# Performance work log

Measured on AMD Instinct MI355X. Metric: run time of the kernel, lower is better.

Reference implementation:

```python
import jax, jax.numpy as jnp
import numpy as np

NC, NPR, E, B = 200000, 100000, 500000, 200000
DIN, HID, HEADS = 16, 256, 8
D = HID // HEADS
NCOLOR, NSIZE, NGROUP = 1000, 30, 50


def setup_inputs() -> dict:
    key = jax.random.key(0)
    ks = jax.random.split(key, 24)
    g = lambda i, shape, s=0.05: jax.random.normal(ks[i], shape, jnp.float32) * s
    return dict(
        customer_x=g(0, (NC, DIN), 1.0),
        product_x=g(1, (NPR, DIN), 1.0),
        proj_cust_W=g(2, (DIN, HID)), proj_cust_b=jnp.zeros((HID,), jnp.float32),
        proj_prod_W=g(3, (DIN, HID)), proj_prod_b=jnp.zeros((HID,), jnp.float32),
        att_src_r=g(4, (HEADS, D)), att_dst_r=g(5, (HEADS, D)),
        att_src_rb=g(6, (HEADS, D)), att_dst_rb=g(7, (HEADS, D)),
        q_sem=g(8, (HID,)), k_lin_W=g(9, (HID, HID)), k_lin_b=jnp.zeros((HID,), jnp.float32),
        color_emb=g(10, (NCOLOR, 8), 1.0),
        size_emb=g(11, (NSIZE, 4), 1.0),
        group_emb=g(12, (NGROUP, 4), 1.0),
        fc1_W=g(13, (HID * 2 + 16, 128)), fc1_b=jnp.zeros((128,), jnp.float32),
        fc2_W=g(14, (128, 32)), fc2_b=jnp.zeros((32,), jnp.float32),
        fc3_W=g(15, (32, 1)), fc3_b=jnp.zeros((1,), jnp.float32),
        bn1_gamma=jnp.ones((128,), jnp.float32), bn1_beta=jnp.zeros((128,), jnp.float32),
        bn2_gamma=jnp.ones((32,), jnp.float32), bn2_beta=jnp.zeros((32,), jnp.float32),
        edge_src=jax.random.randint(ks[16], (E,), 0, NC),
        edge_dst=jax.random.randint(ks[17], (E,), 0, NPR),
        label_src=jax.random.randint(ks[18], (B,), 0, NC),
        label_dst=jax.random.randint(ks[19], (B,), 0, NPR),
        size_idx=jax.random.randint(ks[20], (B,), 0, NSIZE),
        color_idx=jax.random.randint(ks[21], (B,), 0, NCOLOR),
        group_idx=jax.random.randint(ks[22], (B,), 0, NGROUP),
    )


def _edge_softmax(logits, dst, n):
    # destination-grouped softmax over edges; logits: [E,H]
    m = jax.ops.segment_max(logits, dst, num_segments=n)
    m = jnp.where(jnp.isfinite(m), m, 0.0)
    e = jnp.exp(logits - m[dst])
    s = jax.ops.segment_sum(e, dst, num_segments=n)
    return e / (s[dst] + 1e-16)


def _han_relation(h_src, h_dst, a_src, a_dst, src, dst, n_dst):
    # h_*: [N,H,D]; a_*: [H,D]
    logits = (h_src * a_src).sum(-1)[src] + (h_dst * a_dst).sum(-1)[dst]  # [E,H]
    logits = jax.nn.leaky_relu(logits, 0.2)
    alpha = _edge_softmax(logits, dst, n_dst)
    msg = alpha[:, :, None] * h_src[src]  # [E,H,D]
    out = jax.ops.segment_sum(msg, dst, num_segments=n_dst)
    return jax.nn.relu(out.reshape(n_dst, -1))  # [N_dst, H*D]


def _group(outs, q, kW, kb):
    # semantic attention over metapaths (PyG HANConv group)
    stk = jnp.stack(outs)  # [M,N,F]
    score = (q * jnp.tanh(stk @ kW + kb).mean(1)).sum(-1)  # [M]
    attn = jax.nn.softmax(score)
    return jnp.einsum('m,mnf->nf', attn, stk)


def _bn(x, gamma, beta):
    mu = x.mean(0)
    var = x.var(0)
    return (x - mu) * jax.lax.rsqrt(var + 1e-5) * gamma + beta


def reference(customer_x, product_x, proj_cust_W, proj_cust_b, proj_prod_W, proj_prod_b,
              att_src_r, att_dst_r, att_src_rb, att_dst_rb, q_sem, k_lin_W, k_lin_b,
              color_emb, size_emb, group_emb, fc1_W, fc1_b, fc2_W, fc2_b, fc3_W, fc3_b,
              bn1_gamma, bn1_beta, bn2_gamma, bn2_beta,
              edge_src, edge_dst, label_src, label_dst, size_idx, color_idx, group_idx):
    h_c = (customer_x @ proj_cust_W + proj_cust_b).reshape(-1, HEADS, D)
    h_p = (product_x @ proj_prod_W + proj_prod_b).reshape(-1, HEADS, D)
    # relation customer -returns-> product
    out_p = _han_relation(h_c, h_p, att_src_r, att_dst_r, edge_src, edge_dst, NPR)
    # relation product -returned_by-> customer (reversed edges)
    out_c = _han_relation(h_p, h_c, att_src_rb, att_dst_rb, edge_dst, edge_src, NC)
    cust = _group([out_c], q_sem, k_lin_W, k_lin_b)  # [NC, 256]
    prod = _group([out_p], q_sem, k_lin_W, k_lin_b)  # [NPR, 256]
    feat = jnp.concatenate([cust[label_src], prod[label_dst],
                            size_emb[size_idx], color_emb[color_idx], group_emb[group_idx]], axis=-1)
    x = jax.nn.relu(feat @ fc1_W + fc1_b)
    x = _bn(x, bn1_gamma, bn1_beta)
    x = jax.nn.relu(x @ fc2_W + fc2_b)
    x = _bn(x, bn2_gamma, bn2_beta)
    return x @ fc3_W + fc3_b
```

## Files before the change

### kernel.cpp

```cpp
#include <hip/hip_runtime.h>

#define NCC 200000
#define NPRR 100000
#define NEE 500000
#define NBB 200000
#define CAPP 96000
#define CAPC 160000

typedef __attribute__((ext_vector_type(8))) short bf16x8;
typedef __attribute__((ext_vector_type(16))) float f32x16;

__device__ __forceinline__ float b2f(unsigned short u){ return __uint_as_float(((unsigned)u)<<16); }
__device__ __forceinline__ unsigned short f2b(float f){
  unsigned x = __float_as_uint(f);
  return (unsigned short)((x + 0x7fffu + ((x>>16)&1u)) >> 16);
}


__global__ __launch_bounds__(256) void wa_prep2(
    const float* __restrict__ Wc, const float* __restrict__ bc,
    const float* __restrict__ attAc, const float* __restrict__ attBc,
    const float* __restrict__ Wp, const float* __restrict__ bp,
    const float* __restrict__ attAp, const float* __restrict__ attBp,
    float* __restrict__ WAc, float* __restrict__ WAp)
{
  int tid = threadIdx.x;
  for (int task = tid; task < 4*17*8; task += 256) {
    int grp = task / 136, rem = task % 136;
    int k = rem >> 3, h = rem & 7;
    const float* att = (grp==0)?attAc:(grp==1)?attBc:(grp==2)?attAp:attBp;
    const float* W   = (grp<2)?Wc:Wp;
    const float* bias= (grp<2)?bc:bp;
    const float* row = (k < 16) ? (W + k*256) : bias;
    float acc = 0.f;
    for (int d = 0; d < 32; d++) acc = fmaf(row[h*32+d], att[h*32+d], acc);
    if (grp<2) WAc[(grp&1)*136 + rem] = acc;
    else       WAp[(grp&1)*136 + rem] = acc;
  }
}

__global__ __launch_bounds__(256) void prep_proj(
    const float* __restrict__ Wc, const float* __restrict__ Wp,
    const float* __restrict__ WAc, const float* __restrict__ WAp,
    unsigned short* __restrict__ WtC, unsigned short* __restrict__ WtP,
    unsigned short* __restrict__ WAtC, unsigned short* __restrict__ WAtP)
{
  int idx = blockIdx.x*256 + threadIdx.x;
  if (idx < 4096){ int n=idx>>4, k=idx&15; WtC[idx]=f2b(Wc[k*256+n]); }
  else if (idx < 8192){ int t=idx-4096; int n=t>>4, k=t&15; WtP[t]=f2b(Wp[k*256+n]); }
  else if (idx < 8704){ int t=idx-8192; int n=t>>4, k=t&15;
    WAtC[t] = (n<16)? f2b(WAc[(n>>3)*136 + k*8 + (n&7)]) : (unsigned short)0; }
  else if (idx < 9216){ int t=idx-8704; int n=t>>4, k=t&15;
    WAtP[t] = (n<16)? f2b(WAp[(n>>3)*136 + k*8 + (n&7)]) : (unsigned short)0; }
}

__global__ __launch_bounds__(256) void prep_fc1(const float* __restrict__ fc1W,
    const float* __restrict__ fc1b,
    const float* __restrict__ size_emb, const float* __restrict__ color_emb,
    const float* __restrict__ group_emb,
    unsigned short* __restrict__ BtC, unsigned short* __restrict__ BtP,
    float* __restrict__ Ts, float* __restrict__ Tc, float* __restrict__ Tg)
{
  int idx = blockIdx.x*256 + threadIdx.x;
  if (idx < 32768){
    int n = idx>>8, k = idx&255;
    BtC[idx] = f2b(fc1W[k*128 + n]);
  } else if (idx < 65536){
    int t = idx - 32768;
    int n = t>>8, k = t&255;
    BtP[t] = f2b(fc1W[(256+k)*128 + n]);
  } else if (idx < 65536 + 30*128){
    int t = idx - 65536;
    int s = t>>7, j = t&127;
    float a = fc1b[j];
    #pragma unroll
    for (int c=0;c<4;c++) a = fmaf(size_emb[s*4+c], fc1W[(512+c)*128+j], a);
    Ts[t] = a;
  } else if (idx < 65536 + 30*128 + 1000*128){
    int t = idx - 65536 - 30*128;
    int col = t>>7, j = t&127;
    float a = 0.f;
    #pragma unroll
    for (int c=0;c<8;c++) a = fmaf(color_emb[col*8+c], fc1W[(516+c)*128+j], a);
    Tc[t] = a;
  } else if (idx < 65536 + 30*128 + 1000*128 + 50*128){
    int t = idx - 65536 - 30*128 - 1000*128;
    int g = t>>7, j = t&127;
    float a = 0.f;
    #pragma unroll
    for (int c=0;c<4;c++) a = fmaf(group_emb[g*4+c], fc1W[(524+c)*128+j], a);
    Tg[t] = a;
  }
}

#define PROJ_NB 2048
__global__ __launch_bounds__(256) void proj_hist(const float* __restrict__ X,
    const unsigned short* __restrict__ Wt, const unsigned short* __restrict__ WAt,
    const float* __restrict__ WA,
    unsigned short* __restrict__ H, float* __restrict__ sA, float* __restrict__ sB,
    int nt, int nHist,
    const int* __restrict__ src, const int* __restrict__ dst,
    int* __restrict__ cnt_c, int* __restrict__ cnt_p, int E,
    const int* __restrict__ lsrc, const int* __restrict__ ldst,
    int* __restrict__ used_c, int* __restrict__ used_p, int B)
{
  __shared__ unsigned short wt[4608];
  __shared__ float biasS[16];
  int tid = threadIdx.x;
  int bid = blockIdx.x;
  int both = 2*nHist;
  bool isHist; int rid;
  if (bid < both){ isHist = (bid & 1); rid = bid >> 1; }
  else           { isHist = false;    rid = nHist + (bid - both); }
  if (isHist){
    int e = rid*256 + tid;
    if (e < E){
      atomicAdd(&cnt_p[dst[e]], 1);
      atomicAdd(&cnt_c[src[e]], 1);
    }
    if (e < B){
      used_c[lsrc[e]] = 1;
      used_p[ldst[e]] = 1;
    }
    return;
  }
  for (int i=tid; i<512; i+=256) ((uint4*)wt)[i] = ((const uint4*)Wt)[i];
  for (int i=tid; i<64;  i+=256) ((uint4*)(wt+4096))[i] = ((const uint4*)WAt)[i];
  if (tid < 16) biasS[tid] = WA[(tid>>3)*136 + 128 + (tid&7)];
  __syncthreads();
  int wv = tid>>6, lane = tid&63, m = lane&31, hi = lane>>5;
  for (int t = rid; t < nt; t += PROJ_NB){
    int node = t*32 + m;
    bf16x8 a;
    {
      const float4* xr = (const float4*)(X + (long long)node*16 + hi*8);
      float4 f0 = xr[0], f1 = xr[1];
      unsigned short av[8] = {f2b(f0.x),f2b(f0.y),f2b(f0.z),f2b(f0.w),
                              f2b(f1.x),f2b(f1.y),f2b(f1.z),f2b(f1.w)};
      a = *(bf16x8*)av;
    }
    #pragma unroll
    for (int s=0;s<2;s++){
      int c0 = wv*64 + s*32;
      bf16x8 b = *(const bf16x8*)(wt + (c0+m)*16 + hi*8);
      f32x16 acc;
      #pragma unroll
      for (int i=0;i<16;i++) acc[i]=0.f;
      acc = __builtin_amdgcn_mfma_f32_32x32x16_bf16(a, b, acc, 0, 0, 0);
      #pragma unroll
      for (int reg=0; reg<16; reg++){
        int row = (reg&3) + 8*(reg>>2) + 4*hi;
        H[(long long)(t*32+row)*256 + c0 + m] = f2b(acc[reg]);
      }
    }
    if (wv == 0){
      bf16x8 b = *(const bf16x8*)(wt + 4096 + m*16 + hi*8);
      f32x16 acc;
      #pragma unroll
      for (int i=0;i<16;i++) acc[i]=0.f;
      acc = __builtin_amdgcn_mfma_f32_32x32x16_bf16(a, b, acc, 0, 0, 0);
      if (m < 16){
        float bias = biasS[m];
        float* dst2 = (m < 8) ? sA : sB;
        int h = m & 7;
        #pragma unroll
        for (int reg=0; reg<16; reg++){
          int row = (reg&3) + 8*(reg>>2) + 4*hi;
          dst2[(long long)(t*32+row)*8 + h] = acc[reg] + bias;
        }
      }
    }
  }
}

__global__ __launch_bounds__(256) void scan_p1f(const int* __restrict__ cnt_p, int* __restrict__ bsum_p, int Np,
    const int* __restrict__ cnt_c, int* __restrict__ bsum_c, int Nc, int BP, int BC,
    const int* __restrict__ used_p, const int* __restrict__ used_c, int* __restrict__ L, int nComp)
{
  __shared__ int red[256];
  __shared__ int hcnt[16];
  int tid = threadIdx.x;
  int bid = blockIdx.x;
  if (bid >= BP + BC){
    int blk2 = bid - (BP + BC);
    int n = blk2*256 + tid;
    if (tid < 16) hcnt[tid] = 0;
    __syncthreads();
    if (n < Np && used_p[n]){
      int b = min((cnt_p[n]+3)>>2, 7);
      atomicAdd(&hcnt[b], 1);
    }
    if (n < Nc && used_c[n]){
      int b = min((cnt_c[n]+3)>>2, 7);
      atomicAdd(&hcnt[8+b], 1);
    }
    __syncthreads();
    if (tid < 8       && hcnt[tid])  atomicAdd(&L[8+tid],      hcnt[tid]);
    else if (tid < 16 && hcnt[tid])  atomicAdd(&L[16+(tid-8)], hcnt[tid]);
    return;
  }
  const int* cnt; int* bsum; int N; int blk;
  if (bid < BP){ cnt=cnt_p; bsum=bsum_p; N=Np; blk=bid; }
  else         { cnt=cnt_c; bsum=bsum_c; N=Nc; blk=bid-BP; }
  int base = blk*1024 + tid*4;
  int s = 0;
  #pragma unroll
  for (int k=0;k<4;k++){ int i=base+k; if (i<N) s += cnt[i]; }
  red[tid] = s;
  __syncthreads();
  for (int off=128; off>0; off>>=1){ if (tid<off) red[tid]+=red[tid+off]; __syncthreads(); }
  if (tid==0) bsum[blk] = red[0];
}

__global__ __launch_bounds__(256) void scan_p2f(int* __restrict__ bsum_p, int Bp, int* __restrict__ rowptr_p, int Np,
    int* __restrict__ bsum_c, int Bc, int* __restrict__ rowptr_c, int Nc, int* __restrict__ L)
{
  __shared__ int ts[256];
  int tid = threadIdx.x;
  if (blockIdx.x == 2){
    if (tid == 0){
      int s = 0;
      #pragma unroll
      for (int b=0;b<8;b++){ L[24+b] = s; s += L[8+b]; }
      L[0] = s;
      s = 0;
      #pragma unroll
      for (int b=0;b<8;b++){ L[32+b] = s; s += L[16+b]; }
      L[1] = s;
    }
    return;
  }
  int* bsum; int B; int* rowptr; int N;
  if (blockIdx.x == 0){ bsum=bsum_p; B=Bp; rowptr=rowptr_p; N=Np; }
  else                { bsum=bsum_c; B=Bc; rowptr=rowptr_c; N=Nc; }
  int v = (tid<B) ? bsum[tid] : 0;
  ts[tid] = v;
  __syncthreads();
  for (int off=1; off<256; off<<=1){
    int t = (tid>=off) ? ts[tid-off] : 0;
    __syncthreads();
    ts[tid] += t;
    __syncthreads();
  }
  if (tid < B) bsum[tid] = ts[tid] - v;
  if (tid == B-1) rowptr[N] = ts[tid];
}

__global__ __launch_bounds__(256) void scan_p3f(const int* __restrict__ cnt_p, const int* __restrict__ bsum_p,
    int* __restrict__ rowptr_p, int Np,
    const int* __restrict__ cnt_c, const int* __restrict__ bsum_c,
    int* __restrict__ rowptr_c, int Nc, int BP)
{
  __shared__ int ts[256];
  const int* cnt; const int* bsum; int* rowptr; int N; int blk;
  if ((int)blockIdx.x < BP){ cnt=cnt_p; bsum=bsum_p; rowptr=rowptr_p; N=Np; blk=blockIdx.x; }
  else                     { cnt=cnt_c; bsum=bsum_c; rowptr=rowptr_c; N=Nc; blk=blockIdx.x-BP; }
  int tid = threadIdx.x;
  int base = blk*1024 + tid*4;
  int v[4]; int s = 0;
  #pragma unroll
  for (int k=0;k<4;k++){ int i=base+k; v[k] = (i<N) ? cnt[i] : 0; s += v[k]; }
  ts[tid] = s;
  __syncthreads();
  for (int off=1; off<256; off<<=1){
    int t = (tid>=off) ? ts[tid-off] : 0;
    __syncthreads();
    ts[tid] += t;
    __syncthreads();
  }
  int run = bsum[blk] + ts[tid] - s;
  #pragma unroll
  for (int k=0;k<4;k++){ int i=base+k; if (i<N){ rowptr[i]=run; run += v[k]; } }
}

__global__ __launch_bounds__(256) void mega2(
    const int* __restrict__ src, const int* __restrict__ dst,
    const int* __restrict__ rp_r, const int* __restrict__ rp_rb,
    int* __restrict__ cnt_p2, int* __restrict__ cnt_c2,
    int* __restrict__ si_r, int* __restrict__ si_rb, int E,
    const int* __restrict__ used_p, const int* __restrict__ rowptr_p, int Np,
    int4* __restrict__ list_p, int* __restrict__ L, int* __restrict__ smap_p,
    const int* __restrict__ used_c, const int* __restrict__ rowptr_c, int Nc,
    int4* __restrict__ list_c, int* __restrict__ smap_c,
    int nComp,
    const float* __restrict__ X, const unsigned short* __restrict__ Wt,
    const unsigned short* __restrict__ WAt, const float* __restrict__ WA,
    unsigned short* __restrict__ H, float* __restrict__ sA, float* __restrict__ sB,
    int nt, int nProj)
{
  __shared__ unsigned short wt[4608];
  __shared__ float biasS[16];
  __shared__ int hcnt[16];
  __shared__ int hbase[16];
  __shared__ int hcur[16];
  int tid = threadIdx.x, bid = blockIdx.x;
  int nB = nComp + nProj;
  int both = 2*nB;
  bool isB; int rid;
  if (bid < both){ isB = (bid & 1); rid = bid >> 1; }
  else           { isB = false;     rid = nB + (bid - both); }
  if (isB){
    if (rid < nComp){
      int n = rid*256 + tid;
      if (tid < 16){ hcnt[tid] = 0; hcur[tid] = 0; }
      __syncthreads();
      int bp = -1, bc = -1;
      int e0p=0,e1p=0,e0c=0,e1c=0;
      if (n < Np && used_p[n]){
        e0p = rowptr_p[n]; e1p = rowptr_p[n+1];
        bp = min(((e1p-e0p)+3)>>2, 7);
        atomicAdd(&hcnt[bp], 1);
      }
      if (n < Nc && used_c[n]){
        e0c = rowptr_c[n]; e1c = rowptr_c[n+1];
        bc = min(((e1c-e0c)+3)>>2, 7);
        atomicAdd(&hcnt[8+bc], 1);
      }
      __syncthreads();
      if (tid < 8)        hbase[tid] = hcnt[tid] ? atomicAdd(&L[64+tid],     hcnt[tid]) : 0;
      else if (tid < 16)  hbase[tid] = hcnt[tid] ? atomicAdd(&L[72+(tid-8)], hcnt[tid]) : 0;
      __syncthreads();
      if (bp >= 0){
        int r = atomicAdd(&hcur[bp], 1);
        int slot = L[24+bp] + hbase[bp] + r;
        if (slot < CAPP){ list_p[slot] = make_int4(n, e0p, e1p, 0); smap_p[n] = slot; }
      }
      if (bc >= 0){
        int r = atomicAdd(&hcur[8+bc], 1);
        int slot = L[32+bc] + hbase[8+bc] + r;
        if (slot < CAPC){ list_c[slot] = make_int4(n, e0c, e1c, 0); smap_c[n] = slot; }
      }
      return;
    }
    int pid = rid - nComp;
    for (int i=tid; i<512; i+=256) ((uint4*)wt)[i] = ((const uint4*)Wt)[i];
    for (int i=tid; i<64;  i+=256) ((uint4*)(wt+4096))[i] = ((const uint4*)WAt)[i];
    if (tid < 16) biasS[tid] = WA[(tid>>3)*136 + 128 + (tid&7)];
    __syncthreads();
    int wv = tid>>6, lane = tid&63, m = lane&31, hi = lane>>5;
    for (int t = pid; t < nt; t += nProj){
      int node = t*32 + m;
      bf16x8 a;
      {
        const float4* xr = (const float4*)(X + (long long)node*16 + hi*8);
        float4 f0 = xr[0], f1 = xr[1];
        unsigned short av[8] = {f2b(f0.x),f2b(f0.y),f2b(f0.z),f2b(f0.w),
                                f2b(f1.x),f2b(f1.y),f2b(f1.z),f2b(f1.w)};
        a = *(bf16x8*)av;
      }
      #pragma unroll
      for (int s=0;s<2;s++){
        int c0 = wv*64 + s*32;
        bf16x8 b = *(const bf16x8*)(wt + (c0+m)*16 + hi*8);
        f32x16 acc;
        #pragma unroll
        for (int i=0;i<16;i++) acc[i]=0.f;
        acc = __builtin_amdgcn_mfma_f32_32x32x16_bf16(a, b, acc, 0, 0, 0);
        #pragma unroll
        for (int reg=0; reg<16; reg++){
          int row = (reg&3) + 8*(reg>>2) + 4*hi;
          H[(long long)(t*32+row)*256 + c0 + m] = f2b(acc[reg]);
        }
      }
      if (wv == 0){
        bf16x8 b = *(const bf16x8*)(wt + 4096 + m*16 + hi*8);
        f32x16 acc;
        #pragma unroll
        for (int i=0;i<16;i++) acc[i]=0.f;
        acc = __builtin_amdgcn_mfma_f32_32x32x16_bf16(a, b, acc, 0, 0, 0);
        if (m < 16){
          float bias = biasS[m];
          float* dst2 = (m < 8) ? sA : sB;
          int h = m & 7;
          #pragma unroll
          for (int reg=0; reg<16; reg++){
            int row = (reg&3) + 8*(reg>>2) + 4*hi;
            dst2[(long long)(t*32+row)*8 + h] = acc[reg] + bias;
          }
        }
      }
    }
    return;
  }
  int e = rid*256 + tid;
  if (e < E){
    int s = src[e], d = dst[e];
    si_r [rp_r [d] + atomicAdd(&cnt_p2[d], 1)] = s;
    si_rb[rp_rb[s] + atomicAdd(&cnt_c2[s], 1)] = d;
  }
}

__device__ __forceinline__ void agg_block(
    const int4* __restrict__ list, int cnt, int base,
    const int* __restrict__ srcidx,
    const float* __restrict__ sSrc, const float* __restrict__ sDst,
    const unsigned short* __restrict__ H, const unsigned short* __restrict__ Bt,
    unsigned short* __restrict__ Y, int tid, unsigned short* feat)
{
  int wv = tid>>6, lane = tid&63;
  int g = lane>>4, ln = lane&15, h = ln>>1;
  #pragma unroll
  for (int t=0;t<2;t++){
    int r = wv*8 + t*4 + g;
    int slot = base + r;
    float acc[16];
    #pragma unroll
    for (int c=0;c<16;c++) acc[c]=0.f;
    float den = 0.f;
    int node = -1, e0 = 0, e1 = 0;
    if (slot < cnt){
      int4 L = list[slot];
      node = L.x; e0 = L.y; e1 = L.z;
    }
    if (node >= 0 && e1 > e0){
      int elast = e1 - 1;
      float sdh = sDst[(long long)node*8 + h];
      for (int e = e0; e < e1; e += 4){
        int i1 = min(e+1, elast), i2 = min(e+2, elast), i3 = min(e+3, elast);
        int s0 = srcidx[e],  s1 = srcidx[i1];
        int s2 = srcidx[i2], s3 = srcidx[i3];
        const uint4* p0 = (const uint4*)&H[(long long)s0*256 + ln*16];
        const uint4* p1 = (const uint4*)&H[(long long)s1*256 + ln*16];
        const uint4* p2 = (const uint4*)&H[(long long)s2*256 + ln*16];
        const uint4* p3 = (const uint4*)&H[(long long)s3*256 + ln*16];
        uint4 uA0 = p0[0], uA1 = p0[1];
        uint4 uB0 = p1[0], uB1 = p1[1];
        uint4 uC0 = p2[0], uC1 = p2[1];
        uint4 uD0 = p3[0], uD1 = p3[1];
        float l0 = sSrc[(long long)s0*8 + h];
        float l1 = sSrc[(long long)s1*8 + h];
        float l2 = sSrc[(long long)s2*8 + h];
        float l3 = sSrc[(long long)s3*8 + h];
        l0 += sdh; l1 += sdh; l2 += sdh; l3 += sdh;
        float w0 = __expf(l0 > 0.f ? l0 : 0.2f*l0);
        float w1 = (e+1 < e1) ? __expf(l1 > 0.f ? l1 : 0.2f*l1) : 0.f;
        float w2 = (e+2 < e1) ? __expf(l2 > 0.f ? l2 : 0.2f*l2) : 0.f;
        float w3 = (e+3 < e1) ? __expf(l3 > 0.f ? l3 : 0.2f*l3) : 0.f;
        den += (w0 + w1) + (w2 + w3);
        unsigned ua[8] = {uA0.x,uA0.y,uA0.z,uA0.w, uA1.x,uA1.y,uA1.z,uA1.w};
        unsigned ub[8] = {uB0.x,uB0.y,uB0.z,uB0.w, uB1.x,uB1.y,uB1.z,uB1.w};
        unsigned uc[8] = {uC0.x,uC0.y,uC0.z,uC0.w, uC1.x,uC1.y,uC1.z,uC1.w};
        unsigned ud[8] = {uD0.x,uD0.y,uD0.z,uD0.w, uD1.x,uD1.y,uD1.z,uD1.w};
        #pragma unroll
        for (int p=0;p<8;p++){
          acc[p*2]   = fmaf(w0, b2f((unsigned short)(ua[p]&0xffffu)), acc[p*2]);
          acc[p*2+1] = fmaf(w0, b2f((unsigned short)(ua[p]>>16)),     acc[p*2+1]);
          acc[p*2]   = fmaf(w1, b2f((unsigned short)(ub[p]&0xffffu)), acc[p*2]);
          acc[p*2+1] = fmaf(w1, b2f((unsigned short)(ub[p]>>16)),     acc[p*2+1]);
          acc[p*2]   = fmaf(w2, b2f((unsigned short)(uc[p]&0xffffu)), acc[p*2]);
          acc[p*2+1] = fmaf(w2, b2f((unsigned short)(uc[p]>>16)),     acc[p*2+1]);
          acc[p*2]   = fmaf(w3, b2f((unsigned short)(ud[p]&0xffffu)), acc[p*2]);
          acc[p*2+1] = fmaf(w3, b2f((unsigned short)(ud[p]>>16)),     acc[p*2+1]);
        }
      }
    }
    float inv = 1.f/(den + 1e-16f);
    unsigned short ov[16];
    #pragma unroll
    for (int c=0;c<16;c++) ov[c] = f2b(fmaxf(acc[c]*inv, 0.f));
    *(uint4*)&feat[r*264 + ln*16]     = *(uint4*)&ov[0];
    *(uint4*)&feat[r*264 + ln*16 + 8] = *(uint4*)&ov[8];
  }
  __syncthreads();
  int m = lane&31, hi = lane>>5;
  f32x16 acc;
  #pragma unroll
  for (int i=0;i<16;i++) acc[i]=0.f;
  const unsigned short* ap  = feat + m*264 + hi*8;
  const unsigned short* btp = Bt + (wv*32 + m)*256 + hi*8;
  #pragma unroll 4
  for (int ks=0; ks<16; ks++){
    bf16x8 a = *(const bf16x8*)(ap + ks*16);
    bf16x8 b = *(const bf16x8*)(btp + ks*16);
    acc = __builtin_amdgcn_mfma_f32_32x32x16_bf16(a, b, acc, 0, 0, 0);
  }
  int col = wv*32 + m;
  #pragma unroll
  for (int reg=0; reg<16; reg++){
    int row = (reg&3) + 8*(reg>>2) + 4*hi;
    Y[(long long)(base+row)*128 + col] = f2b(acc[reg]);
  }
}

__global__ __launch_bounds__(256) void agg2(
    const int4* __restrict__ listP, const int* __restrict__ lcntP,
    const int* __restrict__ siR,
    const float* __restrict__ sCr, const float* __restrict__ sPr,
    const unsigned short* __restrict__ Hc, const unsigned short* __restrict__ BtP,
    unsigned short* __restrict__ YP, int nP,
    const int4* __restrict__ listC, const int* __restrict__ lcntC,
    const int* __restrict__ siRB,
    const float* __restrict__ sPrb, const float* __restrict__ sCrb,
    const unsigned short* __restrict__ Hp, const unsigned short* __restrict__ BtC,
    unsigned short* __restrict__ YC)
{
  __shared__ unsigned short feat[32*264];
  int bid = blockIdx.x, tid = threadIdx.x;
  int both = 2*nP;
  bool isR; int rid;
  if (bid < both){ isR = !(bid & 1); rid = bid >> 1; }
  else           { isR = false;      rid = nP + (bid - both); }
  if (isR){
    int cnt = *lcntP;
    int base = rid*32;
    if (base >= cnt) return;
    agg_block(listP, cnt, base, siR, sCr, sPr, Hc, BtP, YP, tid, feat);
  } else {
    int cnt = *lcntC;
    int base = rid*32;
    if (base >= cnt) return;
    agg_block(listC, cnt, base, siRB, sPrb, sCrb, Hp, BtC, YC, tid, feat);
  }
}

__global__ __launch_bounds__(256) void gather_fc1(
    const unsigned short* __restrict__ Yc, const unsigned short* __restrict__ Yp,
    const int* __restrict__ smap_c, const int* __restrict__ smap_p,
    const float* __restrict__ Ts, const float* __restrict__ Tc, const float* __restrict__ Tg,
    const int* __restrict__ lsrc, const int* __restrict__ ldst,
    const int* __restrict__ sidx, const int* __restrict__ cidx, const int* __restrict__ gidx,
    unsigned short* __restrict__ x1, float* __restrict__ bnsum, int ntiles)
{
  __shared__ float redS[16][128];
  __shared__ float redQ[16][128];
  int tid = threadIdx.x;
  int rl = tid>>4, g = tid&15;
  float sacc[8] = {0,0,0,0,0,0,0,0};
  float qacc[8] = {0,0,0,0,0,0,0,0};
  for (int t = blockIdx.x; t < ntiles; t += gridDim.x){
    long long row = (long long)t*16 + rl;
    int ls = smap_c[lsrc[row]], ld = smap_p[ldst[row]];
    int si = sidx[row], ci = cidx[row], gi = gidx[row];
    uint4 uc = *(const uint4*)&Yc[(long long)ls*128 + g*8];
    uint4 up = *(const uint4*)&Yp[(long long)ld*128 + g*8];
    float4 t0 = *(const float4*)&Ts[si*128 + g*8];
    float4 t1 = *(const float4*)&Ts[si*128 + g*8 + 4];
    float4 c0 = *(const float4*)&Tc[ci*128 + g*8];
    float4 c1 = *(const float4*)&Tc[ci*128 + g*8 + 4];
    float4 g0 = *(const float4*)&Tg[gi*128 + g*8];
    float4 g1 = *(const float4*)&Tg[gi*128 + g*8 + 4];
    unsigned ucs[4] = {uc.x,uc.y,uc.z,uc.w};
    unsigned ups[4] = {up.x,up.y,up.z,up.w};
    float tb[8] = {t0.x+c0.x+g0.x, t0.y+c0.y+g0.y, t0.z+c0.z+g0.z, t0.w+c0.w+g0.w,
                   t1.x+c1.x+g1.x, t1.y+c1.y+g1.y, t1.z+c1.z+g1.z, t1.w+c1.w+g1.w};
    unsigned short ov[8];
    #pragma unroll
    for (int p=0;p<4;p++){
      float vl = b2f((unsigned short)(ucs[p]&0xffffu)) + b2f((unsigned short)(ups[p]&0xffffu)) + tb[p*2];
      float vh = b2f((unsigned short)(ucs[p]>>16))     + b2f((unsigned short)(ups[p]>>16))     + tb[p*2+1];
      vl = fmaxf(vl, 0.f); vh = fmaxf(vh, 0.f);
      ov[p*2] = f2b(vl); ov[p*2+1] = f2b(vh);
      sacc[p*2]   += vl; qacc[p*2]   += vl*vl;
      sacc[p*2+1] += vh; qacc[p*2+1] += vh*vh;
    }
    *(uint4*)&x1[row*128 + g*8] = *(uint4*)ov;
  }
  #pragma unroll
  for (int j=0;j<8;j++){ redS[rl][g*8+j]=sacc[j]; redQ[rl][g*8+j]=qacc[j]; }
  __syncthreads();
  if (tid < 128){
    float s=0.f, q=0.f;
    #pragma unroll
    for (int r=0;r<16;r++){ s += redS[r][tid]; q += redQ[r][tid]; }
    atomicAdd(&bnsum[tid], s);
    atomicAdd(&bnsum[128+tid], q);
  }
}

__global__ void bn1_fold(const float* __restrict__ bnsum,
    const float* __restrict__ gamma, const float* __restrict__ beta,
    const float* __restrict__ fc2W, const float* __restrict__ fc2b,
    unsigned short* __restrict__ Bt2, float* __restrict__ b2p, float invB)
{
  __shared__ float sc[128], sh[128];
  int tid = threadIdx.x;
  if (tid<128){
    float mu  = bnsum[tid]*invB;
    float var = bnsum[128+tid]*invB - mu*mu;
    float s = gamma[tid] * rsqrtf(var + 1e-5f);
    sc[tid]=s; sh[tid]= beta[tid] - mu*s;
  }
  __syncthreads();
  for (int idx=tid; idx<32*128; idx+=256){
    int n = idx>>7, k = idx&127;
    Bt2[idx] = f2b(sc[k]*fc2W[k*32+n]);
  }
  if (tid<32){
    float a = fc2b[tid];
    for (int k=0;k<128;k++) a = fmaf(sh[k], fc2W[k*32+tid], a);
    b2p[tid]=a;
  }
}

__global__ __launch_bounds__(256) void fc2_mfma(const unsigned short* __restrict__ x1,
    const unsigned short* __restrict__ Bt2, const float* __restrict__ b2p,
    unsigned short* __restrict__ x2, float* __restrict__ bnsum2, int M)
{
  __shared__ unsigned short xt[128*136];
  __shared__ unsigned short wt[32*136];
  __shared__ float redS[4][32];
  __shared__ float redQ[4][32];
  int tid = threadIdx.x;
  long long base = (long long)blockIdx.x*128;
  for (int idx=tid; idx<128*16; idx+=256){
    int r = idx>>4, c = idx&15;
    uint4 u = make_uint4(0,0,0,0);
    if (base + r < M) u = *(const uint4*)&x1[(base+r)*128 + c*8];
    *(uint4*)&xt[r*136 + c*8] = u;
  }
  for (int idx=tid; idx<32*16; idx+=256){
    int r = idx>>4, c = idx&15;
    *(uint4*)&wt[r*136 + c*8] = *(const uint4*)&Bt2[r*128 + c*8];
  }
  __syncthreads();
  int wv = tid>>6, lane = tid&63;
  int m = lane&31, hi = lane>>5;
  f32x16 acc;
  #pragma unroll
  for (int i=0;i<16;i++) acc[i]=0.f;
  const unsigned short* ap = xt + (wv*32 + m)*136 + hi*8;
  const unsigned short* bp = wt + m*136 + hi*8;
  #pragma unroll
  for (int ks=0; ks<8; ks++){
    bf16x8 a = *(const bf16x8*)(ap + ks*16);
    bf16x8 b = *(const bf16x8*)(bp + ks*16);
    acc = __builtin_amdgcn_mfma_f32_32x32x16_bf16(a, b, acc, 0, 0, 0);
  }
  int col = m;
  float bias = b2p[col];
  float s=0.f, q=0.f;
  #pragma unroll
  for (int reg=0; reg<16; reg++){
    int row = (reg&3) + 8*(reg>>2) + 4*hi;
    long long grow = base + wv*32 + row;
    float v = fmaxf(acc[reg] + bias, 0.f);
    if (grow < M) x2[grow*32 + col] = f2b(v);
    s += v; q += v*v;
  }
  if (base + 128 > M){
    s = 0.f; q = 0.f;
    #pragma unroll
    for (int reg=0; reg<16; reg++){
      int row = (reg&3) + 8*(reg>>2) + 4*hi;
      long long grow = base + wv*32 + row;
      float v = fmaxf(acc[reg] + bias, 0.f);
      if (grow < M){ s += v; q += v*v; }
    }
  }
  s += __shfl_xor(s, 32);
  q += __shfl_xor(q, 32);
  if (hi == 0){ redS[wv][col] = s; redQ[wv][col] = q; }
  __syncthreads();
  if (tid < 32){
    float a = redS[0][tid]+redS[1][tid]+redS[2][tid]+redS[3][tid];
    float b = redQ[0][tid]+redQ[1][tid]+redQ[2][tid]+redQ[3][tid];
    atomicAdd(&bnsum2[tid], a);
    atomicAdd(&bnsum2[32+tid], b);
  }
}

__global__ void bn2_fold(const float* __restrict__ bnsum2,
    const float* __restrict__ gamma2, const float* __restrict__ beta2,
    const float* __restrict__ fc3W, const float* __restrict__ fc3b,
    float* __restrict__ w3p, float invB)
{
  __shared__ float sh3[32];
  int tid = threadIdx.x;
  if (tid<32){
    float mu  = bnsum2[tid]*invB;
    float var = bnsum2[32+tid]*invB - mu*mu;
    float s   = gamma2[tid] * rsqrtf(var + 1e-5f);
    float shv = beta2[tid] - mu*s;
    float w   = fc3W[tid];
    w3p[tid]  = s*w;
    sh3[tid]  = shv*w;
  }
  __syncthreads();
  if (tid==0){
    float a = fc3b[0];
    for (int j=0;j<32;j++) a += sh3[j];
    w3p[32] = a;
  }
}

__global__ __launch_bounds__(256) void fc3_kernel(const unsigned short* __restrict__ x2,
    const float* __restrict__ w3p, float* __restrict__ out)
{
  __shared__ float wl[34];
  int tid = threadIdx.x;
  if (tid<33) wl[tid]=w3p[tid];
  __syncthreads();
  long long row = (long long)blockIdx.x*32 + (tid>>3);
  int j0 = (tid&7)*4;
  uint2 u = *(const uint2*)(x2 + row*32 + j0);
  float a = b2f((unsigned short)(u.x&0xffffu))*wl[j0]
          + b2f((unsigned short)(u.x>>16))   *wl[j0+1]
          + b2f((unsigned short)(u.y&0xffffu))*wl[j0+2]
          + b2f((unsigned short)(u.y>>16))   *wl[j0+3];
  a += __shfl_xor(a,1);
  a += __shfl_xor(a,2);
  a += __shfl_xor(a,4);
  if ((tid&7)==0) out[row] = a + wl[32];
}

extern "C" void kernel_launch(void* const* d_in, const int* in_sizes, int n_in,
                              void* d_out, int out_size, void* d_ws, size_t ws_size,
                              hipStream_t stream)
{
  (void)in_sizes; (void)n_in; (void)out_size; (void)ws_size;
  const float* customer_x = (const float*)d_in[0];
  const float* product_x  = (const float*)d_in[1];
  const float* pcW = (const float*)d_in[2];
  const float* pcB = (const float*)d_in[3];
  const float* ppW = (const float*)d_in[4];
  const float* ppB = (const float*)d_in[5];
  const float* att_src_r  = (const float*)d_in[6];
  const float* att_dst_r  = (const float*)d_in[7];
  const float* att_src_rb = (const float*)d_in[8];
  const float* att_dst_rb = (const float*)d_in[9];
  const float* color_emb = (const float*)d_in[13];
  const float* size_emb  = (const float*)d_in[14];
  const float* group_emb = (const float*)d_in[15];
  const float* fc1W = (const float*)d_in[16];
  const float* fc1b = (const float*)d_in[17];
  const float* fc2W = (const float*)d_in[18];
  const float* fc2b = (const float*)d_in[19];
  const float* fc3W = (const float*)d_in[20];
  const float* fc3b = (const float*)d_in[21];
  const float* bn1g = (const float*)d_in[22];
  const float* bn1b = (const float*)d_in[23];
  const float* bn2g = (const float*)d_in[24];
  const float* bn2b = (const float*)d_in[25];
  const int* edge_src  = (const int*)d_in[26];
  const int* edge_dst  = (const int*)d_in[27];
  const int* label_src = (const int*)d_in[28];
  const int* label_dst = (const int*)d_in[29];
  const int* size_idx  = (const int*)d_in[30];
  const int* color_idx = (const int*)d_in[31];
  const int* group_idx = (const int*)d_in[32];

  char* ws = (char*)d_ws;
  size_t off = 0;
  auto alloc = [&](size_t bytes)->char* {
    char* p = ws + off;
    off += (bytes + 255) & ~(size_t)255;
    return p;
  };
  unsigned short* H_c  = (unsigned short*)alloc((size_t)NCC*256*2);
  unsigned short* H_p  = (unsigned short*)alloc((size_t)NPRR*256*2);
  unsigned short* Y_p  = (unsigned short*)alloc((size_t)CAPP*128*2);
  unsigned short* Y_c  = (unsigned short*)alloc((size_t)CAPC*128*2);
  float* s_cr     = (float*)alloc((size_t)NCC*8*4);
  float* s_crb    = (float*)alloc((size_t)NCC*8*4);
  float* s_pr     = (float*)alloc((size_t)NPRR*8*4);
  float* s_prb    = (float*)alloc((size_t)NPRR*8*4);
  int* rowptr_r   = (int*)alloc((size_t)(NPRR+1)*4);
  int* rowptr_rb  = (int*)alloc((size_t)(NCC+1)*4);
  int* srcidx_r   = (int*)alloc((size_t)NEE*4);
  int* srcidx_rb  = (int*)alloc((size_t)NEE*4);
  int* cnts       = (int*)alloc((size_t)(NCC+NPRR)*3*4);
  int* cnt_c      = cnts;
  int* cnt_p      = cnts + NCC;
  int* cnt_c2     = cnts + NCC + NPRR;
  int* cnt_p2     = cnts + NCC + NPRR + NCC;
  int* used_c     = cnts + (NCC + NPRR)*2;
  int* used_p     = used_c + NCC;
  int* smap_p     = (int*)alloc((size_t)NPRR*4);
  int* smap_c     = (int*)alloc((size_t)NCC*4);
  int* bsum_c     = (int*)alloc(256*4);
  int* bsum_p     = (int*)alloc(256*4);
  int4* list_p    = (int4*)alloc((size_t)CAPP*16);
  int4* list_c    = (int4*)alloc((size_t)CAPC*16);
  int* lcnt       = (int*)alloc(512);
  unsigned short* BtC = (unsigned short*)alloc(128*256*2);
  unsigned short* BtP = (unsigned short*)alloc(128*256*2);
  float* Ts     = (float*)alloc(30*128*4);
  float* Tc     = (float*)alloc(1000*128*4);
  float* Tg     = (float*)alloc(50*128*4);
  float* wa_c   = (float*)alloc(272*4);
  float* wa_p   = (float*)alloc(272*4);
  unsigned short* WtC  = (unsigned short*)alloc(256*16*2);
  unsigned short* WtP  = (unsigned short*)alloc(256*16*2);
  unsigned short* WAtC = (unsigned short*)alloc(32*16*2);
  unsigned short* WAtP = (unsigned short*)alloc(32*16*2);
  float* bnsum1 = (float*)alloc(256*4);
  float* bnsum2 = (float*)alloc(64*4);
  unsigned short* Bt2 = (unsigned short*)alloc(32*128*2);
  float* b2p    = (float*)alloc(32*4);
  float* w3p    = (float*)alloc(34*4);
  unsigned short* x1b = H_p;
  unsigned short* x2b = (unsigned short*)s_cr;

  hipMemsetAsync(bnsum1, 0, 1280, stream);
  hipMemsetAsync(cnts, 0, (size_t)(NCC+NPRR)*3*4, stream);
  hipMemsetAsync(lcnt, 0, 512, stream);

  wa_prep2<<<1,256,0,stream>>>(pcW, pcB, att_src_r, att_dst_rb,
                               ppW, ppB, att_dst_r, att_src_rb, wa_c, wa_p);
  prep_proj<<<36,256,0,stream>>>(pcW, ppW, wa_c, wa_p, WtC, WtP, WAtC, WAtP);
  prep_fc1<<<(203776+255)/256,256,0,stream>>>(fc1W, fc1b, size_emb, color_emb, group_emb,
      BtC, BtP, Ts, Tc, Tg);

  const int eg = (NEE+255)/256;
  const int BP = (NPRR+1023)/1024;
  const int BC = (NCC +1023)/1024;
  const int nComp = (NCC+255)/256;
  const int nProjP = 1024;
  const int nP = CAPP/32;
  const int nC = CAPC/32;

  proj_hist<<<PROJ_NB+eg,256,0,stream>>>(customer_x, WtC, WAtC, wa_c,
      H_c, s_cr, s_crb, NCC/32, eg,
      edge_src, edge_dst, cnt_c, cnt_p, NEE,
      label_src, label_dst, used_c, used_p, NBB);

  scan_p1f<<<BP+BC+nComp,256,0,stream>>>(cnt_p, bsum_p, NPRR, cnt_c, bsum_c, NCC, BP, BC,
      used_p, used_c, lcnt, nComp);
  scan_p2f<<<3,256,0,stream>>>(bsum_p, BP, rowptr_r, NPRR, bsum_c, BC, rowptr_rb, NCC, lcnt);
  scan_p3f<<<BP+BC,256,0,stream>>>(cnt_p, bsum_p, rowptr_r, NPRR,
      cnt_c, bsum_c, rowptr_rb, NCC, BP);

  mega2<<<eg + (nComp+nProjP),256,0,stream>>>(edge_src, edge_dst,
      rowptr_r, rowptr_rb, cnt_p2, cnt_c2, srcidx_r, srcidx_rb, NEE,
      used_p, rowptr_r, NPRR, list_p, lcnt, smap_p,
      used_c, rowptr_rb, NCC, list_c, smap_c, nComp,
      product_x, WtP, WAtP, wa_p, H_p, s_pr, s_prb, NPRR/32, nProjP);

  agg2<<<nP+nC,256,0,stream>>>(list_p, &lcnt[0], srcidx_r, s_cr, s_pr, H_c, BtP, Y_p, nP,
                               list_c, &lcnt[1], srcidx_rb, s_prb, s_crb, H_p, BtC, Y_c);

  gather_fc1<<<2048,256,0,stream>>>(Y_c, Y_p, smap_c, smap_p, Ts, Tc, Tg,
      label_src, label_dst, size_idx, color_idx, group_idx, x1b, bnsum1, NBB/16);

  bn1_fold<<<1,256,0,stream>>>(bnsum1, bn1g, bn1b, fc2W, fc2b, Bt2, b2p, 1.0f/NBB);
  fc2_mfma<<<(NBB+127)/128,256,0,stream>>>(x1b, Bt2, b2p, x2b, bnsum2, NBB);
  bn2_fold<<<1,64,0,stream>>>(bnsum2, bn2g, bn2b, fc3W, fc3b, w3p, 1.0f/NBB);
  fc3_kernel<<<NBB/32,256,0,stream>>>(x2b, w3p, (float*)d_out);
}
```

Before: 530.1 us.

## Record per-edge atomic ranks in histogram pass and unroll aggregation by eight

The histogram pass now stores the return value of its atomic increments as a per-edge rank. The CSR fill step can then place each edge directly without a second round of atomics, and the second count arrays and part of the memset go away. The aggregation loop also gains a fast path for nodes with at most four edges, and unrolls by eight for larger degrees to raise memory-level parallelism in the gathers. The cost is two extra 2 MB rank arrays written and read back, and higher register pressure from the 8-wide unroll.

```diff
diff --git a/kernel.cpp b/kernel.cpp
--- a/kernel.cpp
+++ b/kernel.cpp
@@ -101,6 +101,7 @@
     int nt, int nHist,
     const int* __restrict__ src, const int* __restrict__ dst,
     int* __restrict__ cnt_c, int* __restrict__ cnt_p, int E,
+    int* __restrict__ rank_r, int* __restrict__ rank_rb,
     const int* __restrict__ lsrc, const int* __restrict__ ldst,
     int* __restrict__ used_c, int* __restrict__ used_p, int B)
 {
@@ -115,8 +116,8 @@
   if (isHist){
     int e = rid*256 + tid;
     if (e < E){
-      atomicAdd(&cnt_p[dst[e]], 1);
-      atomicAdd(&cnt_c[src[e]], 1);
+      rank_r [e] = atomicAdd(&cnt_p[dst[e]], 1);
+      rank_rb[e] = atomicAdd(&cnt_c[src[e]], 1);
     }
     if (e < B){
       used_c[lsrc[e]] = 1;
@@ -276,7 +277,7 @@
 __global__ __launch_bounds__(256) void mega2(
     const int* __restrict__ src, const int* __restrict__ dst,
     const int* __restrict__ rp_r, const int* __restrict__ rp_rb,
-    int* __restrict__ cnt_p2, int* __restrict__ cnt_c2,
+    const int* __restrict__ rank_r, const int* __restrict__ rank_rb,
     int* __restrict__ si_r, int* __restrict__ si_rb, int E,
     const int* __restrict__ used_p, const int* __restrict__ rowptr_p, int Np,
     int4* __restrict__ list_p, int* __restrict__ L, int* __restrict__ smap_p,
@@ -385,8 +386,8 @@
   int e = rid*256 + tid;
   if (e < E){
     int s = src[e], d = dst[e];
-    si_r [rp_r [d] + atomicAdd(&cnt_p2[d], 1)] = s;
-    si_rb[rp_rb[s] + atomicAdd(&cnt_c2[s], 1)] = d;
+    si_r [rp_r [d] + rank_r [e]] = s;
+    si_rb[rp_rb[s] + rank_rb[e]] = d;
   }
 }
 
@@ -412,10 +413,12 @@
       int4 L = list[slot];
       node = L.x; e0 = L.y; e1 = L.z;
     }
-    if (node >= 0 && e1 > e0){
+    int deg = e1 - e0;
+    if (node >= 0 && deg > 0){
       int elast = e1 - 1;
       float sdh = sDst[(long long)node*8 + h];
-      for (int e = e0; e < e1; e += 4){
+      if (deg <= 4){
+        int e = e0;
         int i1 = min(e+1, elast), i2 = min(e+2, elast), i3 = min(e+3, elast);
         int s0 = srcidx[e],  s1 = srcidx[i1];
         int s2 = srcidx[i2], s3 = srcidx[i3];
@@ -427,11 +430,10 @@
         uint4 uB0 = p1[0], uB1 = p1[1];
         uint4 uC0 = p2[0], uC1 = p2[1];
         uint4 uD0 = p3[0], uD1 = p3[1];
-        float l0 = sSrc[(long long)s0*8 + h];
-        float l1 = sSrc[(long long)s1*8 + h];
-        float l2 = sSrc[(long long)s2*8 + h];
-        float l3 = sSrc[(long long)s3*8 + h];
-        l0 += sdh; l1 += sdh; l2 += sdh; l3 += sdh;
+        float l0 = sSrc[(long long)s0*8 + h] + sdh;
+        float l1 = sSrc[(long long)s1*8 + h] + sdh;
+        float l2 = sSrc[(long long)s2*8 + h] + sdh;
+        float l3 = sSrc[(long long)s3*8 + h] + sdh;
         float w0 = __expf(l0 > 0.f ? l0 : 0.2f*l0);
         float w1 = (e+1 < e1) ? __expf(l1 > 0.f ? l1 : 0.2f*l1) : 0.f;
         float w2 = (e+2 < e1) ? __expf(l2 > 0.f ? l2 : 0.2f*l2) : 0.f;
@@ -451,6 +453,77 @@
           acc[p*2+1] = fmaf(w2, b2f((unsigned short)(uc[p]>>16)),     acc[p*2+1]);
           acc[p*2]   = fmaf(w3, b2f((unsigned short)(ud[p]&0xffffu)), acc[p*2]);
           acc[p*2+1] = fmaf(w3, b2f((unsigned short)(ud[p]>>16)),     acc[p*2+1]);
+        }
+      } else {
+        for (int e = e0; e < e1; e += 8){
+          int i1 = min(e+1, elast), i2 = min(e+2, elast), i3 = min(e+3, elast);
+          int i4 = min(e+4, elast), i5 = min(e+5, elast), i6 = min(e+6, elast), i7 = min(e+7, elast);
+          int s0 = srcidx[e],  s1 = srcidx[i1], s2 = srcidx[i2], s3 = srcidx[i3];
+          int s4 = srcidx[i4], s5 = srcidx[i5], s6 = srcidx[i6], s7 = srcidx[i7];
+          const uint4* p0 = (const uint4*)&H[(long long)s0*256 + ln*16];
+          const uint4* p1 = (const uint4*)&H[(long long)s1*256 + ln*16];
+          const uint4* p2 = (const uint4*)&H[(long long)s2*256 + ln*16];
+          const uint4* p3 = (const uint4*)&H[(long long)s3*256 + ln*16];
+          const uint4* p4 = (const uint4*)&H[(long long)s4*256 + ln*16];
+          const uint4* p5 = (const uint4*)&H[(long long)s5*256 + ln*16];
+          const uint4* p6 = (const uint4*)&H[(long long)s6*256 + ln*16];
+          const uint4* p7 = (const uint4*)&H[(long long)s7*256 + ln*16];
+          uint4 uA0 = p0[0], uA1 = p0[1];
+          uint4 uB0 = p1[0], uB1 = p1[1];
+          uint4 uC0 = p2[0], uC1 = p2[1];
+          uint4 uD0 = p3[0], uD1 = p3[1];
+          uint4 uE0 = p4[0], uE1 = p4[1];
+          uint4 uF0 = p5[0], uF1 = p5[1];
+          uint4 uG0 = p6[0], uG1 = p6[1];
+          uint4 uI0 = p7[0], uI1 = p7[1];
+          float l0 = sSrc[(long long)s0*8 + h] + sdh;
+          float l1 = sSrc[(long long)s1*8 + h] + sdh;
+          float l2 = sSrc[(long long)s2*8 + h] + sdh;
+          float l3 = sSrc[(long long)s3*8 + h] + sdh;
+          float l4 = sSrc[(long long)s4*8 + h] + sdh;
+          float l5 = sSrc[(long long)s5*8 + h] + sdh;
+          float l6 = sSrc[(long long)s6*8 + h] + sdh;
+          float l7 = sSrc[(long long)s7*8 + h] + sdh;
+          float w0 = __expf(l0 > 0.f ? l0 : 0.2f*l0);
+          float w1 = (e+1 < e1) ? __expf(l1 > 0.f ? l1 : 0.2f*l1) : 0.f;
+          float w2 = (e+2 < e1) ? __expf(l2 > 0.f ? l2 : 0.2f*l2) : 0.f;
+          float w3 = (e+3 < e1) ? __expf(l3 > 0.f ? l3 : 0.2f*l3) : 0.f;
+          float w4 = (e+4 < e1) ? __expf(l4 > 0.f ? l4 : 0.2f*l4) : 0.f;
+          float w5 = (e+5 < e1) ? __expf(l5 > 0.f ? l5 : 0.2f*l5) : 0.f;
+          float w6 = (e+6 < e1) ? __expf(l6 > 0.f ? l6 : 0.2f*l6) : 0.f;
+          float w7 = (e+7 < e1) ? __expf(l7 > 0.f ? l7 : 0.2f*l7) : 0.f;
+          den += (w0 + w1) + (w2 + w3);
+          den += (w4 + w5) + (w6 + w7);
+          unsigned ua[8] = {uA0.x,uA0.y,uA0.z,uA0.w, uA1.x,uA1.y,uA1.z,uA1.w};
+          unsigned ub[8] = {uB0.x,uB0.y,uB0.z,uB0.w, uB1.x,uB1.y,uB1.z,uB1.w};
+          unsigned uc[8] = {uC0.x,uC0.y,uC0.z,uC0.w, uC1.x,uC1.y,uC1.z,uC1.w};
+          unsigned ud[8] = {uD0.x,uD0.y,uD0.z,uD0.w, uD1.x,uD1.y,uD1.z,uD1.w};
+          unsigned ue[8] = {uE0.x,uE0.y,uE0.z,uE0.w, uE1.x,uE1.y,uE1.z,uE1.w};
+          unsigned uf[8] = {uF0.x,uF0.y,uF0.z,uF0.w, uF1.x,uF1.y,uF1.z,uF1.w};
+          unsigned ug[8] = {uG0.x,uG0.y,uG0.z,uG0.w, uG1.x,uG1.y,uG1.z,uG1.w};
+          unsigned ui[8] = {uI0.x,uI0.y,uI0.z,uI0.w, uI1.x,uI1.y,uI1.z,uI1.w};
+          #pragma unroll
+          for (int p=0;p<8;p++){
+            acc[p*2]   = fmaf(w0, b2f((unsigned short)(ua[p]&0xffffu)), acc[p*2]);
+            acc[p*2+1] = fmaf(w0, b2f((unsigned short)(ua[p]>>16)),     acc[p*2+1]);
+            acc[p*2]   = fmaf(w1, b2f((unsigned short)(ub[p]&0xffffu)), acc[p*2]);
+            acc[p*2+1] = fmaf(w1, b2f((unsigned short)(ub[p]>>16)),     acc[p*2+1]);
+            acc[p*2]   = fmaf(w2, b2f((unsigned short)(uc[p]&0xffffu)), acc[p*2]);
+            acc[p*2+1] = fmaf(w2, b2f((unsigned short)(uc[p]>>16)),     acc[p*2+1]);
+            acc[p*2]   = fmaf(w3, b2f((unsigned short)(ud[p]&0xffffu)), acc[p*2]);
+            acc[p*2+1] = fmaf(w3, b2f((unsigned short)(ud[p]>>16)),     acc[p*2+1]);
+          }
+          #pragma unroll
+          for (int p=0;p<8;p++){
+            acc[p*2]   = fmaf(w4, b2f((unsigned short)(ue[p]&0xffffu)), acc[p*2]);
+            acc[p*2+1] = fmaf(w4, b2f((unsigned short)(ue[p]>>16)),     acc[p*2+1]);
+            acc[p*2]   = fmaf(w5, b2f((unsigned short)(uf[p]&0xffffu)), acc[p*2]);
+            acc[p*2+1] = fmaf(w5, b2f((unsigned short)(uf[p]>>16)),     acc[p*2+1]);
+            acc[p*2]   = fmaf(w6, b2f((unsigned short)(ug[p]&0xffffu)), acc[p*2]);
+            acc[p*2+1] = fmaf(w6, b2f((unsigned short)(ug[p]>>16)),     acc[p*2+1]);
+            acc[p*2]   = fmaf(w7, b2f((unsigned short)(ui[p]&0xffffu)), acc[p*2]);
+            acc[p*2+1] = fmaf(w7, b2f((unsigned short)(ui[p]>>16)),     acc[p*2+1]);
+          }
         }
       }
     }
@@ -758,12 +831,12 @@
   int* rowptr_rb  = (int*)alloc((size_t)(NCC+1)*4);
   int* srcidx_r   = (int*)alloc((size_t)NEE*4);
   int* srcidx_rb  = (int*)alloc((size_t)NEE*4);
-  int* cnts       = (int*)alloc((size_t)(NCC+NPRR)*3*4);
+  int* rank_r     = (int*)alloc((size_t)NEE*4);
+  int* rank_rb    = (int*)alloc((size_t)NEE*4);
+  int* cnts       = (int*)alloc((size_t)(NCC+NPRR)*2*4);
   int* cnt_c      = cnts;
   int* cnt_p      = cnts + NCC;
-  int* cnt_c2     = cnts + NCC + NPRR;
-  int* cnt_p2     = cnts + NCC + NPRR + NCC;
-  int* used_c     = cnts + (NCC + NPRR)*2;
+  int* used_c     = cnts + NCC + NPRR;
   int* used_p     = used_c + NCC;
   int* smap_p     = (int*)alloc((size_t)NPRR*4);
   int* smap_c     = (int*)alloc((size_t)NCC*4);
@@ -792,7 +865,7 @@
   unsigned short* x2b = (unsigned short*)s_cr;
 
   hipMemsetAsync(bnsum1, 0, 1280, stream);
-  hipMemsetAsync(cnts, 0, (size_t)(NCC+NPRR)*3*4, stream);
+  hipMemsetAsync(cnts, 0, (size_t)(NCC+NPRR)*2*4, stream);
   hipMemsetAsync(lcnt, 0, 512, stream);
 
   wa_prep2<<<1,256,0,stream>>>(pcW, pcB, att_src_r, att_dst_rb,
@@ -811,7 +884,7 @@
 
   proj_hist<<<PROJ_NB+eg,256,0,stream>>>(customer_x, WtC, WAtC, wa_c,
       H_c, s_cr, s_crb, NCC/32, eg,
-      edge_src, edge_dst, cnt_c, cnt_p, NEE,
+      edge_src, edge_dst, cnt_c, cnt_p, NEE, rank_r, rank_rb,
       label_src, label_dst, used_c, used_p, NBB);
 
   scan_p1f<<<BP+BC+nComp,256,0,stream>>>(cnt_p, bsum_p, NPRR, cnt_c, bsum_c, NCC, BP, BC,
@@ -821,7 +894,7 @@
       cnt_c, bsum_c, rowptr_rb, NCC, BP);
 
   mega2<<<eg + (nComp+nProjP),256,0,stream>>>(edge_src, edge_dst,
-      rowptr_r, rowptr_rb, cnt_p2, cnt_c2, srcidx_r, srcidx_rb, NEE,
+      rowptr_r, rowptr_rb, rank_r, rank_rb, srcidx_r, srcidx_rb, NEE,
       used_p, rowptr_r, NPRR, list_p, lcnt, smap_p,
       used_c, rowptr_rb, NCC, list_c, smap_c, nComp,
       product_x, WtP, WAtP, wa_p, H_p, s_pr, s_prb, NPRR/32, nProjP);
```

New measurement: 552.9 us. 1.04x slower.
